# Kernel tuning notes

Hardware: AMD Instinct MI355X
Metric: run time of the kernel (lower is better)

## Reference

```python
import jax, jax.numpy as jnp
import numpy as np

B, S, H, F, E, TOPK = 2, 1024, 1024, 2816, 8, 2

def setup_inputs() -> dict:
    key = jax.random.key(0)
    k1, k2, k3, k4 = jax.random.split(key, 4)
    return {
        "hidden_states": jax.random.normal(k1, (B, S, H), dtype=jnp.float32),
        "gate_w": jax.random.normal(k2, (E, H), dtype=jnp.float32) * 0.02,  # gate 1x1 conv == [E,H] matrix
        "w1": jax.random.normal(k3, (E, F, H), dtype=jnp.float32) * 0.02,   # per-expert up-proj
        "w2": jax.random.normal(k4, (E, H, F), dtype=jnp.float32) * 0.02,   # per-expert down-proj
        "top_k": TOPK,
    }

def reference(hidden_states, gate_w, w1, w2, top_k):
    b, s, h = hidden_states.shape
    e = gate_w.shape[0]
    x = hidden_states.reshape(-1, h)                       # [N, H]
    n = x.shape[0]
    # Router: 1x1 conv gate == linear, softmax, top-k, renormalize
    logits = x @ gate_w.T                                  # [N, E]
    probs = jax.nn.softmax(logits, axis=-1)
    topw, topi = jax.lax.top_k(probs, top_k)               # [N, k]
    topw = topw / jnp.sum(topw, axis=-1, keepdims=True)
    # Per-(token, expert) combine weight; zero for non-selected experts.
    # Equivalent to torch.where(topk_indices == e, topk_weights, 0).sum(-1).
    comb = jnp.zeros((n, e), dtype=x.dtype).at[jnp.arange(n)[:, None], topi].add(topw)  # [N, E]
    # Expert MLPs (1x1 convs == GEMMs): up -> SiLU -> down, weighted combine.
    up = jnp.einsum('nh,efh->nef', x, w1)                  # [N, E, F]
    act = jax.nn.silu(up)
    out = jnp.einsum('nef,ehf->neh', act, w2)              # [N, E, H]
    y = jnp.einsum('ne,neh->nh', comb, out)                # weighted combine
    return y.reshape(b, s, h)
```

## Files before the change

kernel.cpp:

```cpp
#include <hip/hip_runtime.h>
#include <hip/hip_bf16.h>
#include <stdint.h>

#define N_TOK 2048
#define H_DIM 1024
#define F_DIM 2816
#define N_EXP 8

#define BK 64
#define LDA 72

typedef __attribute__((ext_vector_type(8))) short bf16x8;
typedef __attribute__((ext_vector_type(4))) float f32x4;

static __device__ __forceinline__ unsigned short f2bf(float f) {
    union { float f; unsigned u; } v; v.f = f;
    unsigned r = v.u + 0x7fffu + ((v.u >> 16) & 1u);
    return (unsigned short)(r >> 16);
}

__global__ __launch_bounds__(256) void router_kernel(
    const float* __restrict__ x, const float* __restrict__ gate_w,
    int* __restrict__ counts, int* __restrict__ row_token, float* __restrict__ row_weight,
    int* __restrict__ slot_e, int* __restrict__ slot_pos)
{
    __shared__ float gsm[N_EXP * H_DIM];
    for (int i = threadIdx.x; i < N_EXP * H_DIM; i += 256) gsm[i] = gate_w[i];
    __syncthreads();

    const int wave = threadIdx.x >> 6;
    const int lane = threadIdx.x & 63;
    const int n = blockIdx.x * 4 + wave;
    if (n >= N_TOK) return;

    float xv[16];
#pragma unroll
    for (int i = 0; i < 16; i++) xv[i] = x[(size_t)n * H_DIM + lane + 64 * i];

    float logit[N_EXP];
#pragma unroll
    for (int e = 0; e < N_EXP; e++) {
        float p = 0.f;
#pragma unroll
        for (int i = 0; i < 16; i++) p += xv[i] * gsm[e * H_DIM + lane + 64 * i];
#pragma unroll
        for (int s = 32; s > 0; s >>= 1) p += __shfl_xor(p, s, 64);
        logit[e] = p;
    }

    if (lane == 0) {
        int e0 = 0; float l0 = logit[0];
#pragma unroll
        for (int e = 1; e < N_EXP; e++) if (logit[e] > l0) { l0 = logit[e]; e0 = e; }
        int e1 = -1; float l1 = -3.4e38f;
#pragma unroll
        for (int e = 0; e < N_EXP; e++) if (e != e0 && logit[e] > l1) { l1 = logit[e]; e1 = e; }
        float w0 = 1.f / (1.f + __expf(l1 - l0));
        float w1 = 1.f - w0;
        int p0 = atomicAdd(&counts[e0], 1);
        int p1 = atomicAdd(&counts[e1], 1);
        row_token[e0 * N_TOK + p0] = n;  row_weight[e0 * N_TOK + p0] = w0;
        row_token[e1 * N_TOK + p1] = n;  row_weight[e1 * N_TOK + p1] = w1;
        slot_e[n * 2 + 0] = e0;  slot_pos[n * 2 + 0] = p0;
        slot_e[n * 2 + 1] = e1;  slot_pos[n * 2 + 1] = p1;
    }
}

__global__ void scan_kernel(const int* __restrict__ counts, int* __restrict__ offsets)
{
    if (threadIdx.x == 0 && blockIdx.x == 0) {
        int acc = 0;
        for (int e = 0; e < N_EXP; e++) { offsets[e] = acc; acc += counts[e]; }
    }
}

__global__ __launch_bounds__(256) void up_gemm_kernel(
    const float* __restrict__ x, const float* __restrict__ w1,
    const int* __restrict__ counts, const int* __restrict__ offsets,
    const int* __restrict__ row_token,
    unsigned short* __restrict__ act)
{
    const int e = blockIdx.z;
    const int cnt = counts[e];
    const int mTile = blockIdx.y;
    if (mTile * 128 >= cnt) return;
    const int fTile = blockIdx.x;
    const int off = offsets[e];

    __shared__ __align__(16) unsigned short As[128 * LDA];
    __shared__ __align__(16) unsigned short Bs[128 * LDA];

    const int tid = threadIdx.x;
    const int lane = tid & 63;
    const int wave = tid >> 6;
    const int wm = (wave >> 1) * 64, wn = (wave & 1) * 64;

    int tokens[8];
#pragma unroll
    for (int j = 0; j < 8; j++) {
        int i = tid + 256 * j;
        int row = i >> 4;
        int pos = mTile * 128 + row;
        tokens[j] = row_token[e * N_TOK + min(pos, cnt - 1)];
    }

    f32x4 acc[4][4];
#pragma unroll
    for (int i = 0; i < 4; i++)
#pragma unroll
        for (int j = 0; j < 4; j++) acc[i][j] = (f32x4)(0.f);

    const float* wbase = w1 + (size_t)e * F_DIM * H_DIM + (size_t)(fTile * 128) * H_DIM;

    for (int kt = 0; kt < H_DIM / BK; kt++) {
        const int k0 = kt * BK;
#pragma unroll
        for (int j = 0; j < 8; j++) {
            int i = tid + 256 * j;
            int row = i >> 4, c = i & 15;
            const float4 v = *(const float4*)(x + (size_t)tokens[j] * H_DIM + k0 + c * 4);
            ushort4 b; b.x = f2bf(v.x); b.y = f2bf(v.y); b.z = f2bf(v.z); b.w = f2bf(v.w);
            *(ushort4*)(As + row * LDA + c * 4) = b;
        }
#pragma unroll
        for (int j = 0; j < 8; j++) {
            int i = tid + 256 * j;
            int row = i >> 4, c = i & 15;
            const float4 v = *(const float4*)(wbase + (size_t)row * H_DIM + k0 + c * 4);
            ushort4 b; b.x = f2bf(v.x); b.y = f2bf(v.y); b.z = f2bf(v.z); b.w = f2bf(v.w);
            *(ushort4*)(Bs + row * LDA + c * 4) = b;
        }
        __syncthreads();
#pragma unroll
        for (int ks = 0; ks < BK / 32; ks++) {
            const int kloc = ks * 32 + (lane >> 4) * 8;
            bf16x8 af[4], bfr[4];
#pragma unroll
            for (int i = 0; i < 4; i++)
                af[i] = *(const bf16x8*)(As + (wm + i * 16 + (lane & 15)) * LDA + kloc);
#pragma unroll
            for (int i = 0; i < 4; i++)
                bfr[i] = *(const bf16x8*)(Bs + (wn + i * 16 + (lane & 15)) * LDA + kloc);
#pragma unroll
            for (int i = 0; i < 4; i++)
#pragma unroll
                for (int j = 0; j < 4; j++)
                    acc[i][j] = __builtin_amdgcn_mfma_f32_16x16x32_bf16(af[i], bfr[j], acc[i][j], 0, 0, 0);
        }
        __syncthreads();
    }

#pragma unroll
    for (int i = 0; i < 4; i++) {
        const int mrow = wm + i * 16 + ((lane >> 4) << 2);
#pragma unroll
        for (int r = 0; r < 4; r++) {
            const int m = mTile * 128 + mrow + r;
            if (m < cnt) {
#pragma unroll
                for (int j = 0; j < 4; j++) {
                    float v = acc[i][j][r];
                    float s = v / (1.f + __expf(-v));
                    int col = fTile * 128 + wn + j * 16 + (lane & 15);
                    act[(size_t)(off + m) * F_DIM + col] = f2bf(s);
                }
            }
        }
    }
}

__global__ __launch_bounds__(256) void down_gemm_kernel(
    const unsigned short* __restrict__ act, const float* __restrict__ w2,
    const int* __restrict__ counts, const int* __restrict__ offsets,
    const float* __restrict__ row_weight,
    float* __restrict__ out_slot)
{
    const int e = blockIdx.z;
    const int cnt = counts[e];
    const int mTile = blockIdx.y;
    if (mTile * 128 >= cnt) return;
    const int hTile = blockIdx.x;
    const int off = offsets[e];

    __shared__ __align__(16) unsigned short As[128 * LDA];
    __shared__ __align__(16) unsigned short Bs[128 * LDA];

    const int tid = threadIdx.x;
    const int lane = tid & 63;
    const int wave = tid >> 6;
    const int wm = (wave >> 1) * 64, wn = (wave & 1) * 64;

    int rowsg[4];
#pragma unroll
    for (int j = 0; j < 4; j++) {
        int i = tid + 256 * j;
        int row = i >> 3;
        rowsg[j] = off + min(mTile * 128 + row, cnt - 1);
    }

    f32x4 acc[4][4];
#pragma unroll
    for (int i = 0; i < 4; i++)
#pragma unroll
        for (int j = 0; j < 4; j++) acc[i][j] = (f32x4)(0.f);

    const float* wbase = w2 + (size_t)e * H_DIM * F_DIM + (size_t)(hTile * 128) * F_DIM;

    for (int kt = 0; kt < F_DIM / BK; kt++) {
        const int k0 = kt * BK;
#pragma unroll
        for (int j = 0; j < 4; j++) {
            int i = tid + 256 * j;
            int row = i >> 3, c = i & 7;
            const uint4 v = *(const uint4*)(act + (size_t)rowsg[j] * F_DIM + k0 + c * 8);
            *(uint4*)(As + row * LDA + c * 8) = v;
        }
#pragma unroll
        for (int j = 0; j < 8; j++) {
            int i = tid + 256 * j;
            int row = i >> 4, c = i & 15;
            const float4 v = *(const float4*)(wbase + (size_t)row * F_DIM + k0 + c * 4);
            ushort4 b; b.x = f2bf(v.x); b.y = f2bf(v.y); b.z = f2bf(v.z); b.w = f2bf(v.w);
            *(ushort4*)(Bs + row * LDA + c * 4) = b;
        }
        __syncthreads();
#pragma unroll
        for (int ks = 0; ks < BK / 32; ks++) {
            const int kloc = ks * 32 + (lane >> 4) * 8;
            bf16x8 af[4], bfr[4];
#pragma unroll
            for (int i = 0; i < 4; i++)
                af[i] = *(const bf16x8*)(As + (wm + i * 16 + (lane & 15)) * LDA + kloc);
#pragma unroll
            for (int i = 0; i < 4; i++)
                bfr[i] = *(const bf16x8*)(Bs + (wn + i * 16 + (lane & 15)) * LDA + kloc);
#pragma unroll
            for (int i = 0; i < 4; i++)
#pragma unroll
                for (int j = 0; j < 4; j++)
                    acc[i][j] = __builtin_amdgcn_mfma_f32_16x16x32_bf16(af[i], bfr[j], acc[i][j], 0, 0, 0);
        }
        __syncthreads();
    }

#pragma unroll
    for (int i = 0; i < 4; i++) {
        const int mrow = wm + i * 16 + ((lane >> 4) << 2);
#pragma unroll
        for (int r = 0; r < 4; r++) {
            const int m = mTile * 128 + mrow + r;
            if (m < cnt) {
                const float w = row_weight[e * N_TOK + m];
#pragma unroll
                for (int j = 0; j < 4; j++) {
                    int col = hTile * 128 + wn + j * 16 + (lane & 15);
                    out_slot[(size_t)(off + m) * H_DIM + col] = w * acc[i][j][r];
                }
            }
        }
    }
}

__global__ __launch_bounds__(256) void combine_kernel(
    const float* __restrict__ out_slot, const int* __restrict__ offsets,
    const int* __restrict__ slot_e, const int* __restrict__ slot_pos,
    float* __restrict__ out)
{
    const int n = blockIdx.x;
    const int r0 = offsets[slot_e[n * 2 + 0]] + slot_pos[n * 2 + 0];
    const int r1 = offsets[slot_e[n * 2 + 1]] + slot_pos[n * 2 + 1];
    const int t = threadIdx.x;
    const float4 a = *(const float4*)(out_slot + (size_t)r0 * H_DIM + t * 4);
    const float4 b = *(const float4*)(out_slot + (size_t)r1 * H_DIM + t * 4);
    float4 c; c.x = a.x + b.x; c.y = a.y + b.y; c.z = a.z + b.z; c.w = a.w + b.w;
    *(float4*)(out + (size_t)n * H_DIM + t * 4) = c;
}

extern "C" void kernel_launch(void* const* d_in, const int* in_sizes, int n_in,
                              void* d_out, int out_size, void* d_ws, size_t ws_size,
                              hipStream_t stream) {
    const float* x      = (const float*)d_in[0];
    const float* gate_w = (const float*)d_in[1];
    const float* w1     = (const float*)d_in[2];
    const float* w2     = (const float*)d_in[3];
    float* out = (float*)d_out;

    char* ws = (char*)d_ws;
    size_t o = 0;
    auto alloc = [&](size_t bytes) -> void* {
        void* p = ws + o;
        o = (o + bytes + 255) & ~(size_t)255;
        return p;
    };
    int*   counts     = (int*)  alloc(N_EXP * sizeof(int));
    int*   offsets    = (int*)  alloc(N_EXP * sizeof(int));
    int*   row_token  = (int*)  alloc((size_t)N_EXP * N_TOK * sizeof(int));
    float* row_weight = (float*)alloc((size_t)N_EXP * N_TOK * sizeof(float));
    int*   slot_e     = (int*)  alloc((size_t)N_TOK * 2 * sizeof(int));
    int*   slot_pos   = (int*)  alloc((size_t)N_TOK * 2 * sizeof(int));
    unsigned short* act = (unsigned short*)alloc((size_t)N_TOK * 2 * F_DIM * sizeof(unsigned short));
    float* out_slot   = (float*)alloc((size_t)N_TOK * 2 * H_DIM * sizeof(float));

    hipMemsetAsync(counts, 0, N_EXP * sizeof(int), stream);

    router_kernel<<<N_TOK / 4, 256, 0, stream>>>(x, gate_w, counts, row_token, row_weight, slot_e, slot_pos);
    scan_kernel<<<1, 64, 0, stream>>>(counts, offsets);
    up_gemm_kernel<<<dim3(F_DIM / 128, N_TOK / 128, N_EXP), 256, 0, stream>>>(
        x, w1, counts, offsets, row_token, act);
    down_gemm_kernel<<<dim3(H_DIM / 128, N_TOK / 128, N_EXP), 256, 0, stream>>>(
        act, w2, counts, offsets, row_weight, out_slot);
    combine_kernel<<<N_TOK, 256, 0, stream>>>(out_slot, offsets, slot_e, slot_pos, out);
}
```

Before: 402.4 us.

## Double-buffer LDS with register prefetch and split-K the down-projection GEMM

After: 447.3 us. 1.11x slower.

```diff
diff --git a/kernel.cpp b/kernel.cpp
--- a/kernel.cpp
+++ b/kernel.cpp
@@ -6,9 +6,12 @@
 #define H_DIM 1024
 #define F_DIM 2816
 #define N_EXP 8
+#define NSLOT (N_TOK * 2)
 
 #define BK 64
 #define LDA 72
+#define KSPLIT 2
+#define KHALF (F_DIM / KSPLIT)
 
 typedef __attribute__((ext_vector_type(8))) short bf16x8;
 typedef __attribute__((ext_vector_type(4))) float f32x4;
@@ -74,7 +77,7 @@
     }
 }
 
-__global__ __launch_bounds__(256) void up_gemm_kernel(
+__global__ __launch_bounds__(256, 2) void up_gemm_kernel(
     const float* __restrict__ x, const float* __restrict__ w1,
     const int* __restrict__ counts, const int* __restrict__ offsets,
     const int* __restrict__ row_token,
@@ -87,8 +90,8 @@
     const int fTile = blockIdx.x;
     const int off = offsets[e];
 
-    __shared__ __align__(16) unsigned short As[128 * LDA];
-    __shared__ __align__(16) unsigned short Bs[128 * LDA];
+    __shared__ __align__(16) unsigned short As[2][128 * LDA];
+    __shared__ __align__(16) unsigned short Bs[2][128 * LDA];
 
     const int tid = threadIdx.x;
     const int lane = tid & 63;
@@ -112,42 +115,56 @@
 
     const float* wbase = w1 + (size_t)e * F_DIM * H_DIM + (size_t)(fTile * 128) * H_DIM;
 
-    for (int kt = 0; kt < H_DIM / BK; kt++) {
-        const int k0 = kt * BK;
+    float4 areg[8], breg[8];
+#pragma unroll
+    for (int j = 0; j < 8; j++) {
+        int i = tid + 256 * j;
+        int row = i >> 4, c = i & 15;
+        areg[j] = *(const float4*)(x + (size_t)tokens[j] * H_DIM + c * 4);
+        breg[j] = *(const float4*)(wbase + (size_t)row * H_DIM + c * 4);
+    }
+
+    const int NKT = H_DIM / BK;
+    for (int kt = 0; kt < NKT; kt++) {
+        const int cur = kt & 1;
 #pragma unroll
         for (int j = 0; j < 8; j++) {
             int i = tid + 256 * j;
             int row = i >> 4, c = i & 15;
-            const float4 v = *(const float4*)(x + (size_t)tokens[j] * H_DIM + k0 + c * 4);
-            ushort4 b; b.x = f2bf(v.x); b.y = f2bf(v.y); b.z = f2bf(v.z); b.w = f2bf(v.w);
-            *(ushort4*)(As + row * LDA + c * 4) = b;
-        }
-#pragma unroll
-        for (int j = 0; j < 8; j++) {
-            int i = tid + 256 * j;
-            int row = i >> 4, c = i & 15;
-            const float4 v = *(const float4*)(wbase + (size_t)row * H_DIM + k0 + c * 4);
-            ushort4 b; b.x = f2bf(v.x); b.y = f2bf(v.y); b.z = f2bf(v.z); b.w = f2bf(v.w);
-            *(ushort4*)(Bs + row * LDA + c * 4) = b;
+            float4 va = areg[j];
+            ushort4 a4; a4.x = f2bf(va.x); a4.y = f2bf(va.y); a4.z = f2bf(va.z); a4.w = f2bf(va.w);
+            *(ushort4*)(As[cur] + row * LDA + c * 4) = a4;
+            float4 vb = breg[j];
+            ushort4 b4; b4.x = f2bf(vb.x); b4.y = f2bf(vb.y); b4.z = f2bf(vb.z); b4.w = f2bf(vb.w);
+            *(ushort4*)(Bs[cur] + row * LDA + c * 4) = b4;
         }
         __syncthreads();
-#pragma unroll
-        for (int ks = 0; ks < BK / 32; ks++) {
-            const int kloc = ks * 32 + (lane >> 4) * 8;
+        if (kt + 1 < NKT) {
+            const int k0 = (kt + 1) * BK;
+#pragma unroll
+            for (int j = 0; j < 8; j++) {
+                int i = tid + 256 * j;
+                int row = i >> 4, c = i & 15;
+                areg[j] = *(const float4*)(x + (size_t)tokens[j] * H_DIM + k0 + c * 4);
+                breg[j] = *(const float4*)(wbase + (size_t)row * H_DIM + k0 + c * 4);
+            }
+        }
+#pragma unroll
+        for (int kk = 0; kk < BK / 32; kk++) {
+            const int kloc = kk * 32 + (lane >> 4) * 8;
             bf16x8 af[4], bfr[4];
 #pragma unroll
             for (int i = 0; i < 4; i++)
-                af[i] = *(const bf16x8*)(As + (wm + i * 16 + (lane & 15)) * LDA + kloc);
-#pragma unroll
-            for (int i = 0; i < 4; i++)
-                bfr[i] = *(const bf16x8*)(Bs + (wn + i * 16 + (lane & 15)) * LDA + kloc);
+                af[i] = *(const bf16x8*)(As[cur] + (wm + i * 16 + (lane & 15)) * LDA + kloc);
+#pragma unroll
+            for (int i = 0; i < 4; i++)
+                bfr[i] = *(const bf16x8*)(Bs[cur] + (wn + i * 16 + (lane & 15)) * LDA + kloc);
 #pragma unroll
             for (int i = 0; i < 4; i++)
 #pragma unroll
                 for (int j = 0; j < 4; j++)
                     acc[i][j] = __builtin_amdgcn_mfma_f32_16x16x32_bf16(af[i], bfr[j], acc[i][j], 0, 0, 0);
         }
-        __syncthreads();
     }
 
 #pragma unroll
@@ -169,21 +186,22 @@
     }
 }
 
-__global__ __launch_bounds__(256) void down_gemm_kernel(
+__global__ __launch_bounds__(256, 2) void down_gemm_kernel(
     const unsigned short* __restrict__ act, const float* __restrict__ w2,
     const int* __restrict__ counts, const int* __restrict__ offsets,
     const float* __restrict__ row_weight,
-    float* __restrict__ out_slot)
-{
-    const int e = blockIdx.z;
+    float* __restrict__ out_partial)
+{
+    const int e  = blockIdx.z & (N_EXP - 1);
+    const int ks = blockIdx.z >> 3;
     const int cnt = counts[e];
     const int mTile = blockIdx.y;
     if (mTile * 128 >= cnt) return;
     const int hTile = blockIdx.x;
     const int off = offsets[e];
 
-    __shared__ __align__(16) unsigned short As[128 * LDA];
-    __shared__ __align__(16) unsigned short Bs[128 * LDA];
+    __shared__ __align__(16) unsigned short As[2][128 * LDA];
+    __shared__ __align__(16) unsigned short Bs[2][128 * LDA];
 
     const int tid = threadIdx.x;
     const int lane = tid & 63;
@@ -205,44 +223,74 @@
         for (int j = 0; j < 4; j++) acc[i][j] = (f32x4)(0.f);
 
     const float* wbase = w2 + (size_t)e * H_DIM * F_DIM + (size_t)(hTile * 128) * F_DIM;
-
-    for (int kt = 0; kt < F_DIM / BK; kt++) {
-        const int k0 = kt * BK;
+    const int kbase = ks * KHALF;
+    const int NKT = KHALF / BK;
+
+    uint4 areg[4]; float4 breg[8];
+#pragma unroll
+    for (int j = 0; j < 4; j++) {
+        int i = tid + 256 * j;
+        int c = i & 7;
+        areg[j] = *(const uint4*)(act + (size_t)rowsg[j] * F_DIM + kbase + c * 8);
+    }
+#pragma unroll
+    for (int j = 0; j < 8; j++) {
+        int i = tid + 256 * j;
+        int row = i >> 4, c = i & 15;
+        breg[j] = *(const float4*)(wbase + (size_t)row * F_DIM + kbase + c * 4);
+    }
+
+    for (int kt = 0; kt < NKT; kt++) {
+        const int cur = kt & 1;
 #pragma unroll
         for (int j = 0; j < 4; j++) {
             int i = tid + 256 * j;
             int row = i >> 3, c = i & 7;
-            const uint4 v = *(const uint4*)(act + (size_t)rowsg[j] * F_DIM + k0 + c * 8);
-            *(uint4*)(As + row * LDA + c * 8) = v;
+            *(uint4*)(As[cur] + row * LDA + c * 8) = areg[j];
         }
 #pragma unroll
         for (int j = 0; j < 8; j++) {
             int i = tid + 256 * j;
             int row = i >> 4, c = i & 15;
-            const float4 v = *(const float4*)(wbase + (size_t)row * F_DIM + k0 + c * 4);
-            ushort4 b; b.x = f2bf(v.x); b.y = f2bf(v.y); b.z = f2bf(v.z); b.w = f2bf(v.w);
-            *(ushort4*)(Bs + row * LDA + c * 4) = b;
+            float4 v = breg[j];
+            ushort4 b4; b4.x = f2bf(v.x); b4.y = f2bf(v.y); b4.z = f2bf(v.z); b4.w = f2bf(v.w);
+            *(ushort4*)(Bs[cur] + row * LDA + c * 4) = b4;
         }
         __syncthreads();
-#pragma unroll
-        for (int ks = 0; ks < BK / 32; ks++) {
-            const int kloc = ks * 32 + (lane >> 4) * 8;
+        if (kt + 1 < NKT) {
+            const int k0 = kbase + (kt + 1) * BK;
+#pragma unroll
+            for (int j = 0; j < 4; j++) {
+                int i = tid + 256 * j;
+                int c = i & 7;
+                areg[j] = *(const uint4*)(act + (size_t)rowsg[j] * F_DIM + k0 + c * 8);
+            }
+#pragma unroll
+            for (int j = 0; j < 8; j++) {
+                int i = tid + 256 * j;
+                int row = i >> 4, c = i & 15;
+                breg[j] = *(const float4*)(wbase + (size_t)row * F_DIM + k0 + c * 4);
+            }
+        }
+#pragma unroll
+        for (int kk = 0; kk < BK / 32; kk++) {
+            const int kloc = kk * 32 + (lane >> 4) * 8;
             bf16x8 af[4], bfr[4];
 #pragma unroll
             for (int i = 0; i < 4; i++)
-                af[i] = *(const bf16x8*)(As + (wm + i * 16 + (lane & 15)) * LDA + kloc);
-#pragma unroll
-            for (int i = 0; i < 4; i++)
-                bfr[i] = *(const bf16x8*)(Bs + (wn + i * 16 + (lane & 15)) * LDA + kloc);
+                af[i] = *(const bf16x8*)(As[cur] + (wm + i * 16 + (lane & 15)) * LDA + kloc);
+#pragma unroll
+            for (int i = 0; i < 4; i++)
+                bfr[i] = *(const bf16x8*)(Bs[cur] + (wn + i * 16 + (lane & 15)) * LDA + kloc);
 #pragma unroll
             for (int i = 0; i < 4; i++)
 #pragma unroll
                 for (int j = 0; j < 4; j++)
                     acc[i][j] = __builtin_amdgcn_mfma_f32_16x16x32_bf16(af[i], bfr[j], acc[i][j], 0, 0, 0);
         }
-        __syncthreads();
-    }
-
+    }
+
+    float* obase = out_partial + (size_t)ks * NSLOT * H_DIM;
 #pragma unroll
     for (int i = 0; i < 4; i++) {
         const int mrow = wm + i * 16 + ((lane >> 4) << 2);
@@ -254,7 +302,7 @@
 #pragma unroll
                 for (int j = 0; j < 4; j++) {
                     int col = hTile * 128 + wn + j * 16 + (lane & 15);
-                    out_slot[(size_t)(off + m) * H_DIM + col] = w * acc[i][j][r];
+                    obase[(size_t)(off + m) * H_DIM + col] = w * acc[i][j][r];
                 }
             }
         }
@@ -262,7 +310,7 @@
 }
 
 __global__ __launch_bounds__(256) void combine_kernel(
-    const float* __restrict__ out_slot, const int* __restrict__ offsets,
+    const float* __restrict__ out_partial, const int* __restrict__ offsets,
     const int* __restrict__ slot_e, const int* __restrict__ slot_pos,
     float* __restrict__ out)
 {
@@ -270,10 +318,18 @@
     const int r0 = offsets[slot_e[n * 2 + 0]] + slot_pos[n * 2 + 0];
     const int r1 = offsets[slot_e[n * 2 + 1]] + slot_pos[n * 2 + 1];
     const int t = threadIdx.x;
-    const float4 a = *(const float4*)(out_slot + (size_t)r0 * H_DIM + t * 4);
-    const float4 b = *(const float4*)(out_slot + (size_t)r1 * H_DIM + t * 4);
-    float4 c; c.x = a.x + b.x; c.y = a.y + b.y; c.z = a.z + b.z; c.w = a.w + b.w;
-    *(float4*)(out + (size_t)n * H_DIM + t * 4) = c;
+    const float* p0 = out_partial;
+    const float* p1 = out_partial + (size_t)NSLOT * H_DIM;
+    const float4 a = *(const float4*)(p0 + (size_t)r0 * H_DIM + t * 4);
+    const float4 b = *(const float4*)(p1 + (size_t)r0 * H_DIM + t * 4);
+    const float4 c = *(const float4*)(p0 + (size_t)r1 * H_DIM + t * 4);
+    const float4 d = *(const float4*)(p1 + (size_t)r1 * H_DIM + t * 4);
+    float4 s;
+    s.x = (a.x + b.x) + (c.x + d.x);
+    s.y = (a.y + b.y) + (c.y + d.y);
+    s.z = (a.z + b.z) + (c.z + d.z);
+    s.w = (a.w + b.w) + (c.w + d.w);
+    *(float4*)(out + (size_t)n * H_DIM + t * 4) = s;
 }
 
 extern "C" void kernel_launch(void* const* d_in, const int* in_sizes, int n_in,
@@ -298,8 +354,8 @@
     float* row_weight = (float*)alloc((size_t)N_EXP * N_TOK * sizeof(float));
     int*   slot_e     = (int*)  alloc((size_t)N_TOK * 2 * sizeof(int));
     int*   slot_pos   = (int*)  alloc((size_t)N_TOK * 2 * sizeof(int));
-    unsigned short* act = (unsigned short*)alloc((size_t)N_TOK * 2 * F_DIM * sizeof(unsigned short));
-    float* out_slot   = (float*)alloc((size_t)N_TOK * 2 * H_DIM * sizeof(float));
+    unsigned short* act = (unsigned short*)alloc((size_t)NSLOT * F_DIM * sizeof(unsigned short));
+    float* out_partial = (float*)alloc((size_t)KSPLIT * NSLOT * H_DIM * sizeof(float));
 
     hipMemsetAsync(counts, 0, N_EXP * sizeof(int), stream);
 
@@ -307,7 +363,7 @@
     scan_kernel<<<1, 64, 0, stream>>>(counts, offsets);
     up_gemm_kernel<<<dim3(F_DIM / 128, N_TOK / 128, N_EXP), 256, 0, stream>>>(
         x, w1, counts, offsets, row_token, act);
-    down_gemm_kernel<<<dim3(H_DIM / 128, N_TOK / 128, N_EXP), 256, 0, stream>>>(
-        act, w2, counts, offsets, row_weight, out_slot);
-    combine_kernel<<<N_TOK, 256, 0, stream>>>(out_slot, offsets, slot_e, slot_pos, out);
-}
+    down_gemm_kernel<<<dim3(H_DIM / 128, N_TOK / 128, N_EXP * KSPLIT), 256, 0, stream>>>(
+        act, w2, counts, offsets, row_weight, out_partial);
+    combine_kernel<<<N_TOK, 256, 0, stream>>>(out_partial, offsets, slot_e, slot_pos, out);
+}
```
